# Kernel optimization log

Measured on AMD Instinct MI355X. Metric: run time of the kernel, lower is better.

## Reference

```python
import jax, jax.numpy as jnp
import numpy as np

DIM = 128
HEADS = 4
HD = DIM // HEADS  # 32
WS = 8             # search window (ws x ws candidates)
K = 16             # top-k neighbors kept
SCALE = HD ** -0.5


def _sepconv(x, w_dw, w_pw, b):
    # depthwise 3x3 ('SAME', reflect-free) + pointwise 1x1 with bias (SepConv2d)
    C = x.shape[1]
    y = jax.lax.conv_general_dilated(x, w_dw, (1, 1), 'SAME',
                                     feature_group_count=C,
                                     dimension_numbers=('NCHW', 'OIHW', 'NCHW'))
    return jnp.einsum('bchw,oc->bohw', y, w_pw) + b[None, :, None, None]


def _refl(i, n):
    # dnls reflect_bounds: mirror indices back into [0, n-1]
    i = jnp.where(i < 0, -i, i)
    return jnp.where(i >= n, 2 * (n - 1) - i, i)


def _neighbor_idx(T, H, W, ws):
    # flat pixel index of the ws*ws spatial candidates per query (wt=0: same frame)
    off = jnp.arange(ws) - ws // 2
    ni = _refl(jnp.arange(H)[:, None] + off[None, :], H)  # [H,ws]
    nj = _refl(jnp.arange(W)[:, None] + off[None, :], W)  # [W,ws]
    pix = ni[:, None, :, None] * W + nj[None, :, None, :]  # [H,W,ws,ws]
    idx = jnp.arange(T)[:, None, None, None, None] * (H * W) + pix[None]
    return idx.reshape(T * H * W, ws * ws).astype(jnp.int32)  # [Q,L]


def reference(vid, wq_dw, wq_pw, bq, wk_dw, wk_pw, bk, wv_dw, wv_pw, bv, proj_w, proj_b):
    B, T, C, H, W = vid.shape
    Q = T * H * W
    x = vid.reshape(B * T, C, H, W)
    # qkv conv projection; q pre-scaled as in get_qkv
    q = _sepconv(x, wq_dw, wq_pw, bq) * SCALE
    k = _sepconv(x, wk_dw, wk_pw, bk)
    v = _sepconv(x, wv_dw, wv_pw, bv)

    def heads(z):  # [B*T,C,H,W] -> [B,heads,Q,hd]
        return z.reshape(B, T, HEADS, HD, H, W).transpose(0, 2, 1, 4, 5, 3).reshape(B, HEADS, Q, HD)

    qh, kh, vh = heads(q), heads(k), heads(v)
    idx = _neighbor_idx(T, H, W, WS)            # [Q,L]
    kg = jnp.take(kh, idx, axis=2)              # [B,h,Q,L,hd] irregular gather
    dists = jnp.einsum('bhqd,bhqld->bhql', qh, kg)
    vals, args = jax.lax.top_k(dists, K)        # k-NN by prod distance
    attn = jax.nn.softmax(vals, axis=-1)        # run_softmax over k
    sel = jnp.take_along_axis(jnp.broadcast_to(idx[None, None], (B, HEADS) + idx.shape), args, axis=-1)
    vsel = jnp.take_along_axis(vh, sel.reshape(B, HEADS, Q * K)[..., None], axis=2).reshape(B, HEADS, Q, K, HD)
    out = jnp.einsum('bhqk,bhqkd->bhqd', attn, vsel)   # wpsum (ps=pt=1)
    out = out.transpose(0, 2, 1, 3).reshape(B, Q, C)   # merge heads: (h c)
    y = out @ proj_w.T + proj_b                        # nn.Linear proj
    # fold: ps=1, stride0=1 -> zvid==1, pure reshape back to video
    return y.reshape(B, T, H, W, C).transpose(0, 1, 4, 2, 3)


def setup_inputs() -> dict:
    key = jax.random.key(0)
    ks = jax.random.split(key, 12)
    s = 0.02
    return {
        'vid': jax.random.normal(ks[0], (1, 2, DIM, 96, 96), jnp.float32),
        'wq_dw': jax.random.normal(ks[1], (DIM, 1, 3, 3), jnp.float32) * s,
        'wq_pw': jax.random.normal(ks[2], (DIM, DIM), jnp.float32) * s,
        'bq': jax.random.normal(ks[3], (DIM,), jnp.float32) * s,
        'wk_dw': jax.random.normal(ks[4], (DIM, 1, 3, 3), jnp.float32) * s,
        'wk_pw': jax.random.normal(ks[5], (DIM, DIM), jnp.float32) * s,
        'bk': jax.random.normal(ks[6], (DIM,), jnp.float32) * s,
        'wv_dw': jax.random.normal(ks[7], (DIM, 1, 3, 3), jnp.float32) * s,
        'wv_pw': jax.random.normal(ks[8], (DIM, DIM), jnp.float32) * s,
        'bv': jax.random.normal(ks[9], (DIM,), jnp.float32) * s,
        'proj_w': jax.random.normal(ks[10], (DIM, DIM), jnp.float32) * s,
        'proj_b': jax.random.normal(ks[11], (DIM,), jnp.float32) * s,
    }
```

## Files before the change

kernel.cpp:

```cpp
#include <hip/hip_runtime.h>
#include <math.h>

#define TT 2
#define CH 128
#define HH 96
#define WW 96
#define HWS 9216
#define QTOT 18432
#define QC (QTOT*CH)
#define HD 32
#define KTOP 16
#define SCALE 0.17677669529663687f

#define SEG 16
#define PR 8
#define PC 23
#define PSTRIDE 36

typedef __attribute__((ext_vector_type(8))) short short8;
typedef __attribute__((ext_vector_type(4))) float floatx4;

__device__ __forceinline__ unsigned short f2bf(float f) {
    union { float f; unsigned u; } x; x.f = f;
    unsigned r = x.u + 0x7fffu + ((x.u >> 16) & 1u);
    return (unsigned short)(r >> 16);
}
__device__ __forceinline__ float bf2f(unsigned short h) {
    return __uint_as_float(((unsigned)h) << 16);
}

__device__ __forceinline__ int refl(int x, int n) {
    x = x < 0 ? -x : x;
    return x >= n ? 2 * (n - 1) - x : x;
}

__global__ __launch_bounds__(256) void dwcvt_kernel(
    const float* __restrict__ x,
    const float* __restrict__ wq, const float* __restrict__ wk, const float* __restrict__ wv,
    unsigned short* __restrict__ qk_hi,
    unsigned short* __restrict__ qk_lo,
    unsigned short* __restrict__ v_bf)
{
    int t = threadIdx.x;
    int pl = t & 63;
    int cg = __builtin_amdgcn_readfirstlane(t >> 6);
    int p  = blockIdx.x * 64 + pl;
    int c0 = blockIdx.y * 32 + cg * 8;
    int hw = p % HWS;
    int tt = p / HWS;
    int i = hw / WW, j = hw % WW;

    unsigned qh[4], ql[4], kh[4], kl[4], vh[4];
#pragma unroll
    for (int ic = 0; ic < 8; ic += 2) {
        float sv[3][2];
#pragma unroll
        for (int u = 0; u < 2; u++) {
            int c = c0 + ic + u;
            const float* xp = x + (size_t)(tt * CH + c) * HWS;
            float w0[9], w1[9], w2[9];
#pragma unroll
            for (int r = 0; r < 9; r++) {
                w0[r] = wq[c * 9 + r]; w1[r] = wk[c * 9 + r]; w2[r] = wv[c * 9 + r];
            }
            float s0 = 0.f, s1 = 0.f, s2 = 0.f;
#pragma unroll
            for (int r = 0; r < 3; r++) {
                int ii = i + r - 1;
                if (ii < 0 || ii >= HH) continue;
#pragma unroll
                for (int ss = 0; ss < 3; ss++) {
                    int jj = j + ss - 1;
                    if (jj < 0 || jj >= WW) continue;
                    float xv = xp[ii * WW + jj];
                    s0 += xv * w0[r * 3 + ss];
                    s1 += xv * w1[r * 3 + ss];
                    s2 += xv * w2[r * 3 + ss];
                }
            }
            sv[0][u] = s0; sv[1][u] = s1; sv[2][u] = s2;
        }
        int w = ic >> 1;
        unsigned short h0 = f2bf(sv[0][0]), h1 = f2bf(sv[0][1]);
        qh[w] = h0 | ((unsigned)h1 << 16);
        ql[w] = f2bf(sv[0][0] - bf2f(h0)) | ((unsigned)f2bf(sv[0][1] - bf2f(h1)) << 16);
        h0 = f2bf(sv[1][0]); h1 = f2bf(sv[1][1]);
        kh[w] = h0 | ((unsigned)h1 << 16);
        kl[w] = f2bf(sv[1][0] - bf2f(h0)) | ((unsigned)f2bf(sv[1][1] - bf2f(h1)) << 16);
        vh[w] = f2bf(sv[2][0]) | ((unsigned)f2bf(sv[2][1]) << 16);
    }
    size_t off = (size_t)p * CH + c0;
    uint4 pk;
    pk.x = qh[0]; pk.y = qh[1]; pk.z = qh[2]; pk.w = qh[3];
    *(uint4*)(qk_hi + off) = pk;
    pk.x = ql[0]; pk.y = ql[1]; pk.z = ql[2]; pk.w = ql[3];
    *(uint4*)(qk_lo + off) = pk;
    pk.x = kh[0]; pk.y = kh[1]; pk.z = kh[2]; pk.w = kh[3];
    *(uint4*)(qk_hi + (size_t)QC + off) = pk;
    pk.x = kl[0]; pk.y = kl[1]; pk.z = kl[2]; pk.w = kl[3];
    *(uint4*)(qk_lo + (size_t)QC + off) = pk;
    pk.x = vh[0]; pk.y = vh[1]; pk.z = vh[2]; pk.w = vh[3];
    *(uint4*)(v_bf + off) = pk;
}

__global__ __launch_bounds__(256) void qk_mfma(
    const unsigned short* __restrict__ Ahi,
    const unsigned short* __restrict__ Alo,
    const float* __restrict__ wq_pw, const float* __restrict__ wk_pw,
    const float* __restrict__ bq, const float* __restrict__ bk,
    float* __restrict__ qkf)
{
    int sel = blockIdx.y;
    const float* W = sel ? wk_pw : wq_pw;
    const float* bias = sel ? bk : bq;
    float scale = sel ? 1.f : SCALE;
    const unsigned short* ah = Ahi + (size_t)sel * QC;
    const unsigned short* al = Alo + (size_t)sel * QC;
    float* O = qkf + (size_t)sel * QC;

    __shared__ unsigned short Wh[128 * 136];
    __shared__ unsigned short Wl[128 * 136];
    int t = threadIdx.x;
#pragma unroll
    for (int r = 0; r < 16; r++) {
        int lin = r * 256 + t;
        int o = lin >> 5, cq = lin & 31;
        float4 w4 = *(const float4*)(W + o * CH + cq * 4);
        unsigned short hx = f2bf(w4.x), hy = f2bf(w4.y), hz = f2bf(w4.z), hw = f2bf(w4.w);
        unsigned short lx = f2bf(w4.x - bf2f(hx)), ly = f2bf(w4.y - bf2f(hy));
        unsigned short lz = f2bf(w4.z - bf2f(hz)), lw = f2bf(w4.w - bf2f(hw));
        uint2 pk;
        pk.x = hx | ((unsigned)hy << 16); pk.y = hz | ((unsigned)hw << 16);
        *(uint2*)(&Wh[o * 136 + cq * 4]) = pk;
        pk.x = lx | ((unsigned)ly << 16); pk.y = lz | ((unsigned)lw << 16);
        *(uint2*)(&Wl[o * 136 + cq * 4]) = pk;
    }
    __syncthreads();
    int wv = t >> 6, lane = t & 63;
    int m = lane & 15, quad = lane >> 4;
    int p0 = blockIdx.x * 64;
    int o0 = wv * 32;
    float bb[2];
#pragma unroll
    for (int ot = 0; ot < 2; ot++) bb[ot] = bias[o0 + ot * 16 + m];
    floatx4 acc[4][2];
#pragma unroll
    for (int i = 0; i < 4; i++)
#pragma unroll
        for (int j = 0; j < 2; j++) acc[i][j] = (floatx4){0.f, 0.f, 0.f, 0.f};
#pragma unroll
    for (int kc = 0; kc < 4; kc++) {
        short8 avh[4], avl[4], bh[2], bl[2];
#pragma unroll
        for (int pt = 0; pt < 4; pt++) {
            size_t base = (size_t)(p0 + pt * 16 + m) * CH + kc * 32 + quad * 8;
            avh[pt] = *(const short8*)(ah + base);
            avl[pt] = *(const short8*)(al + base);
        }
#pragma unroll
        for (int ot = 0; ot < 2; ot++) {
            int lidx = (o0 + ot * 16 + m) * 136 + kc * 32 + quad * 8;
            bh[ot] = *(const short8*)(&Wh[lidx]);
            bl[ot] = *(const short8*)(&Wl[lidx]);
        }
#pragma unroll
        for (int pt = 0; pt < 4; pt++)
#pragma unroll
            for (int ot = 0; ot < 2; ot++) {
                acc[pt][ot] = __builtin_amdgcn_mfma_f32_16x16x32_bf16(avh[pt], bh[ot], acc[pt][ot], 0, 0, 0);
                acc[pt][ot] = __builtin_amdgcn_mfma_f32_16x16x32_bf16(avh[pt], bl[ot], acc[pt][ot], 0, 0, 0);
                acc[pt][ot] = __builtin_amdgcn_mfma_f32_16x16x32_bf16(avl[pt], bh[ot], acc[pt][ot], 0, 0, 0);
            }
    }
#pragma unroll
    for (int pt = 0; pt < 4; pt++)
#pragma unroll
        for (int ot = 0; ot < 2; ot++)
#pragma unroll
            for (int reg = 0; reg < 4; reg++) {
                int p = p0 + pt * 16 + quad * 4 + reg;
                O[(size_t)p * CH + o0 + ot * 16 + m] = (acc[pt][ot][reg] + bb[ot]) * scale;
            }
}

__global__ __launch_bounds__(256) void vgemm_mfma(
    const unsigned short* __restrict__ A,
    const float* __restrict__ W,
    const float* __restrict__ bias,
    float* __restrict__ O)
{
    __shared__ unsigned short Ws[128 * 136];
    int t = threadIdx.x;
#pragma unroll
    for (int r = 0; r < 16; r++) {
        int lin = r * 256 + t;
        int o = lin >> 5, cq = lin & 31;
        float4 w4 = *(const float4*)(W + o * CH + cq * 4);
        uint2 pk;
        pk.x = f2bf(w4.x) | ((unsigned)f2bf(w4.y) << 16);
        pk.y = f2bf(w4.z) | ((unsigned)f2bf(w4.w) << 16);
        *(uint2*)(&Ws[o * 136 + cq * 4]) = pk;
    }
    __syncthreads();
    int wv = t >> 6, lane = t & 63;
    int m = lane & 15, quad = lane >> 4;
    int p0 = blockIdx.x * 64;
    int o0 = wv * 32;
    float bb[2];
#pragma unroll
    for (int ot = 0; ot < 2; ot++) bb[ot] = bias[o0 + ot * 16 + m];
    floatx4 acc[4][2];
#pragma unroll
    for (int i = 0; i < 4; i++)
#pragma unroll
        for (int j = 0; j < 2; j++) acc[i][j] = (floatx4){0.f, 0.f, 0.f, 0.f};
#pragma unroll
    for (int kc = 0; kc < 4; kc++) {
        short8 a[4], b[2];
#pragma unroll
        for (int pt = 0; pt < 4; pt++)
            a[pt] = *(const short8*)(A + (size_t)(p0 + pt * 16 + m) * CH + kc * 32 + quad * 8);
#pragma unroll
        for (int ot = 0; ot < 2; ot++)
            b[ot] = *(const short8*)(&Ws[(o0 + ot * 16 + m) * 136 + kc * 32 + quad * 8]);
#pragma unroll
        for (int pt = 0; pt < 4; pt++)
#pragma unroll
            for (int ot = 0; ot < 2; ot++)
                acc[pt][ot] = __builtin_amdgcn_mfma_f32_16x16x32_bf16(a[pt], b[ot], acc[pt][ot], 0, 0, 0);
    }
#pragma unroll
    for (int pt = 0; pt < 4; pt++)
#pragma unroll
        for (int ot = 0; ot < 2; ot++)
#pragma unroll
            for (int reg = 0; reg < 4; reg++) {
                int p = p0 + pt * 16 + quad * 4 + reg;
                O[(size_t)p * CH + o0 + ot * 16 + m] = acc[pt][ot][reg] + bb[ot];
            }
}

__global__ __launch_bounds__(256) void attn_kernel(
    const float* __restrict__ q,
    const float* __restrict__ k,
    const float* __restrict__ v,
    unsigned short* __restrict__ att)
{
    __shared__ float kp[PR * PC * PSTRIDE];
    int h = blockIdx.y;
    int seg = blockIdx.x;
    int qj0 = (seg % (WW / SEG)) * SEG;
    int qi = (seg / (WW / SEG)) % HH;
    int tt = seg / ((WW / SEG) * HH);
    int t = threadIdx.x;

#pragma unroll
    for (int r = 0; r < 6; r++) {
        int f = r * 256 + t;
        if (f < PR * PC * 8) {
            int pix = f >> 3, d4 = f & 7;
            int ci = pix / PC, cj = pix - ci * PC;
            int gi = refl(qi + ci - 4, HH);
            int gj = refl(qj0 + cj - 4, WW);
            int gp = tt * HWS + gi * WW + gj;
            *(float4*)(&kp[pix * PSTRIDE + d4 * 4]) =
                *(const float4*)(k + (size_t)gp * CH + h * HD + d4 * 4);
        }
    }
    __syncthreads();

    int wv = t >> 6, lane = t & 63;
    int ci = lane >> 3, cjo = lane & 7;
    int di = ci - 4, dj = cjo - 4;
    int rowoff = tt * HWS + refl(qi + di, HH) * WW;
    const int d = lane & (HD - 1);
    const unsigned long long below = (1ull << lane) - 1ull;

    for (int ql = wv * 4; ql < wv * 4 + 4; ql++) {
        int qj = qj0 + ql;
        int p = tt * HWS + qi * WW + qj;
        const float* qp = q + (size_t)p * CH + h * HD;
        const float* kr = &kp[(ci * PC + ql + cjo) * PSTRIDE];
        float dist = 0.f;
#pragma unroll
        for (int dd = 0; dd < 8; dd++) {
            float4 qv = *(const float4*)(qp + dd * 4);
            float4 kv = *(const float4*)(kr + dd * 4);
            dist += qv.x * kv.x + qv.y * kv.y + qv.z * kv.z + qv.w * kv.w;
        }
        int cpix = rowoff + refl(qj + dj, WW);

        unsigned u = __float_as_uint(dist);
        unsigned key = (u & 0x80000000u) ? ~u : (u | 0x80000000u);

        unsigned prefix = 0u;
        int need = KTOP;
#pragma unroll
        for (int bit = 31; bit >= 0; --bit) {
            unsigned hi = (prefix >> bit) | 1u;
            unsigned long long b = __ballot((key >> bit) == hi);
            int cnt = __popcll(b);
            bool take = cnt >= need;
            prefix = take ? (prefix | (1u << bit)) : prefix;
            need = take ? need : need - cnt;
        }
        bool isEq = (key == prefix);
        unsigned long long eqm = __ballot(isEq);
        int rk = __popcll(eqm & below);
        bool selb = (key > prefix) || (isEq && rk < need);
        unsigned long long selm = __ballot(selb);

        float e = selb ? __expf(dist) : 0.f;

        float acc = 0.f, denom = 0.f;
        unsigned long long m0 = selm;
#pragma unroll
        for (int r = 0; r < KTOP; r++) {
            int s0 = __builtin_ctzll(m0); m0 &= m0 - 1ull;
            float a0 = __uint_as_float((unsigned)__builtin_amdgcn_readlane((int)__float_as_uint(e), s0));
            int p0 = __builtin_amdgcn_readlane(cpix, s0);
            denom += a0;
            acc += a0 * v[(size_t)p0 * CH + h * HD + d];
        }
        if (lane < HD)
            att[(size_t)p * CH + h * HD + lane] = f2bf(acc / denom);
    }
}

__global__ __launch_bounds__(256) void proj_mfma(
    const unsigned short* __restrict__ A,
    const float* __restrict__ W,
    const float* __restrict__ bias,
    float* __restrict__ out)
{
    __shared__ unsigned short Ws[128 * 136];
    int t = threadIdx.x;
#pragma unroll
    for (int r = 0; r < 16; r++) {
        int lin = r * 256 + t;
        int o = lin >> 5, cq = lin & 31;
        float4 w4 = *(const float4*)(W + o * CH + cq * 4);
        uint2 pk;
        pk.x = f2bf(w4.x) | ((unsigned)f2bf(w4.y) << 16);
        pk.y = f2bf(w4.z) | ((unsigned)f2bf(w4.w) << 16);
        *(uint2*)(&Ws[o * 136 + cq * 4]) = pk;
    }
    __syncthreads();
    int wv = t >> 6, lane = t & 63;
    int m = lane & 15, quad = lane >> 4;
    int p0 = blockIdx.x * 64;
    int o0 = wv * 32;
    float bb[2][4];
#pragma unroll
    for (int ot = 0; ot < 2; ot++)
#pragma unroll
        for (int reg = 0; reg < 4; reg++) bb[ot][reg] = bias[o0 + ot * 16 + quad * 4 + reg];
    floatx4 acc[2][4];
#pragma unroll
    for (int i = 0; i < 2; i++)
#pragma unroll
        for (int j = 0; j < 4; j++) acc[i][j] = (floatx4){0.f, 0.f, 0.f, 0.f};
#pragma unroll
    for (int kc = 0; kc < 4; kc++) {
        short8 a[2], b[4];
#pragma unroll
        for (int ot = 0; ot < 2; ot++)
            a[ot] = *(const short8*)(&Ws[(o0 + ot * 16 + m) * 136 + kc * 32 + quad * 8]);
#pragma unroll
        for (int pt = 0; pt < 4; pt++)
            b[pt] = *(const short8*)(A + (size_t)(p0 + pt * 16 + m) * CH + kc * 32 + quad * 8);
#pragma unroll
        for (int ot = 0; ot < 2; ot++)
#pragma unroll
            for (int pt = 0; pt < 4; pt++)
                acc[ot][pt] = __builtin_amdgcn_mfma_f32_16x16x32_bf16(a[ot], b[pt], acc[ot][pt], 0, 0, 0);
    }
    int tt = p0 / HWS;
    int hwb = p0 - tt * HWS;
#pragma unroll
    for (int ot = 0; ot < 2; ot++)
#pragma unroll
        for (int pt = 0; pt < 4; pt++)
#pragma unroll
            for (int reg = 0; reg < 4; reg++) {
                int o = o0 + ot * 16 + quad * 4 + reg;
                int hw = hwb + pt * 16 + m;
                out[((size_t)(tt * CH + o)) * HWS + hw] = acc[ot][pt][reg] + bb[ot][reg];
            }
}

extern "C" void kernel_launch(void* const* d_in, const int* in_sizes, int n_in,
                              void* d_out, int out_size, void* d_ws, size_t ws_size,
                              hipStream_t stream) {
    const float* vid    = (const float*)d_in[0];
    const float* wq_dw  = (const float*)d_in[1];
    const float* wq_pw  = (const float*)d_in[2];
    const float* bq     = (const float*)d_in[3];
    const float* wk_dw  = (const float*)d_in[4];
    const float* wk_pw  = (const float*)d_in[5];
    const float* bk     = (const float*)d_in[6];
    const float* wv_dw  = (const float*)d_in[7];
    const float* wv_pw  = (const float*)d_in[8];
    const float* bv     = (const float*)d_in[9];
    const float* proj_w = (const float*)d_in[10];
    const float* proj_b = (const float*)d_in[11];
    float* out = (float*)d_out;

    float* qkf = (float*)d_ws;
    float* v_f32 = qkf + (size_t)2 * QC;
    unsigned short* qk_hi = (unsigned short*)(v_f32 + (size_t)QC);
    unsigned short* qk_lo = qk_hi + (size_t)2 * QC;
    unsigned short* v_bf = qk_lo + (size_t)2 * QC;
    unsigned short* att_bf = v_bf;

    dwcvt_kernel<<<dim3(QTOT / 64, 4), 256, 0, stream>>>(
        vid, wq_dw, wk_dw, wv_dw, qk_hi, qk_lo, v_bf);
    qk_mfma<<<dim3(QTOT / 64, 2), 256, 0, stream>>>(qk_hi, qk_lo, wq_pw, wk_pw, bq, bk, qkf);
    vgemm_mfma<<<QTOT / 64, 256, 0, stream>>>(v_bf, wv_pw, bv, v_f32);
    attn_kernel<<<dim3(TT * HH * (WW / SEG), 4), 256, 0, stream>>>(
        qkf, qkf + (size_t)QC, v_f32, att_bf);
    proj_mfma<<<QTOT / 64, 256, 0, stream>>>(att_bf, proj_w, proj_b, out);
}
```

Before: 206.0 us.

## Fuse V projection into QK GEMM and projection into attention kernel

Merges the V pointwise GEMM into the Q/K GEMM launch as a third grid slice, with a fourth slice pre-converting proj weights to bf16. V is now stored in bf16 in a per-head [h][Q][32] layout, which halves gather traffic and makes the 16 neighbor reads per query contiguous. The attention kernel loops over all four heads per block, keeps the attended row in LDS, and runs the output projection with MFMA directly, removing the att buffer round trip and a launch. In exchange each attention block does four times the serial work with fewer blocks, reloads K tiles per head with extra barriers, and reads proj weights from global memory instead of LDS.

```diff
diff --git a/kernel.cpp b/kernel.cpp
--- a/kernel.cpp
+++ b/kernel.cpp
@@ -50,7 +50,7 @@
     int tt = p / HWS;
     int i = hw / WW, j = hw % WW;
 
-    unsigned qh[4], ql[4], kh[4], kl[4], vh[4];
+    unsigned qh[4], ql[4], kh[4], kl[4], vh4[4];
 #pragma unroll
     for (int ic = 0; ic < 8; ic += 2) {
         float sv[3][2];
@@ -87,7 +87,7 @@
         h0 = f2bf(sv[1][0]); h1 = f2bf(sv[1][1]);
         kh[w] = h0 | ((unsigned)h1 << 16);
         kl[w] = f2bf(sv[1][0] - bf2f(h0)) | ((unsigned)f2bf(sv[1][1] - bf2f(h1)) << 16);
-        vh[w] = f2bf(sv[2][0]) | ((unsigned)f2bf(sv[2][1]) << 16);
+        vh4[w] = f2bf(sv[2][0]) | ((unsigned)f2bf(sv[2][1]) << 16);
     }
     size_t off = (size_t)p * CH + c0;
     uint4 pk;
@@ -99,18 +99,91 @@
     *(uint4*)(qk_hi + (size_t)QC + off) = pk;
     pk.x = kl[0]; pk.y = kl[1]; pk.z = kl[2]; pk.w = kl[3];
     *(uint4*)(qk_lo + (size_t)QC + off) = pk;
-    pk.x = vh[0]; pk.y = vh[1]; pk.z = vh[2]; pk.w = vh[3];
+    pk.x = vh4[0]; pk.y = vh4[1]; pk.z = vh4[2]; pk.w = vh4[3];
     *(uint4*)(v_bf + off) = pk;
 }
 
-__global__ __launch_bounds__(256) void qk_mfma(
+__global__ __launch_bounds__(256) void qkv_mfma(
     const unsigned short* __restrict__ Ahi,
     const unsigned short* __restrict__ Alo,
+    const unsigned short* __restrict__ Avb,
     const float* __restrict__ wq_pw, const float* __restrict__ wk_pw,
-    const float* __restrict__ bq, const float* __restrict__ bk,
-    float* __restrict__ qkf)
+    const float* __restrict__ wv_pw, const float* __restrict__ proj_w,
+    const float* __restrict__ bq, const float* __restrict__ bk, const float* __restrict__ bv,
+    float* __restrict__ qkf,
+    unsigned short* __restrict__ vh,
+    unsigned short* __restrict__ wp_bf)
 {
+    __shared__ unsigned short WhS[128 * 136];
+    __shared__ unsigned short WlS[128 * 136];
     int sel = blockIdx.y;
+    int t = threadIdx.x;
+
+    if (sel == 3) {
+        if (blockIdx.x < 16) {
+            int idx = blockIdx.x * 256 + t;
+            float4 w4 = *(const float4*)(proj_w + idx * 4);
+            uint2 pk;
+            pk.x = f2bf(w4.x) | ((unsigned)f2bf(w4.y) << 16);
+            pk.y = f2bf(w4.z) | ((unsigned)f2bf(w4.w) << 16);
+            *(uint2*)(wp_bf + idx * 4) = pk;
+        }
+        return;
+    }
+
+    int wv = t >> 6, lane = t & 63;
+    int m = lane & 15, quad = lane >> 4;
+    int p0 = blockIdx.x * 64;
+    int o0 = wv * 32;
+
+    if (sel == 2) {
+#pragma unroll
+        for (int r = 0; r < 16; r++) {
+            int lin = r * 256 + t;
+            int o = lin >> 5, cq = lin & 31;
+            float4 w4 = *(const float4*)(wv_pw + o * CH + cq * 4);
+            uint2 pk;
+            pk.x = f2bf(w4.x) | ((unsigned)f2bf(w4.y) << 16);
+            pk.y = f2bf(w4.z) | ((unsigned)f2bf(w4.w) << 16);
+            *(uint2*)(&WhS[o * 136 + cq * 4]) = pk;
+        }
+        __syncthreads();
+        float bb[2];
+#pragma unroll
+        for (int ot = 0; ot < 2; ot++) bb[ot] = bv[o0 + ot * 16 + m];
+        floatx4 acc[4][2];
+#pragma unroll
+        for (int i = 0; i < 4; i++)
+#pragma unroll
+            for (int j = 0; j < 2; j++) acc[i][j] = (floatx4){0.f, 0.f, 0.f, 0.f};
+#pragma unroll
+        for (int kc = 0; kc < 4; kc++) {
+            short8 a[4], b[2];
+#pragma unroll
+            for (int pt = 0; pt < 4; pt++)
+                a[pt] = *(const short8*)(Avb + (size_t)(p0 + pt * 16 + m) * CH + kc * 32 + quad * 8);
+#pragma unroll
+            for (int ot = 0; ot < 2; ot++)
+                b[ot] = *(const short8*)(&WhS[(o0 + ot * 16 + m) * 136 + kc * 32 + quad * 8]);
+#pragma unroll
+            for (int pt = 0; pt < 4; pt++)
+#pragma unroll
+                for (int ot = 0; ot < 2; ot++)
+                    acc[pt][ot] = __builtin_amdgcn_mfma_f32_16x16x32_bf16(a[pt], b[ot], acc[pt][ot], 0, 0, 0);
+        }
+        unsigned short* vhh = vh + (size_t)wv * QTOT * 32;
+#pragma unroll
+        for (int pt = 0; pt < 4; pt++)
+#pragma unroll
+            for (int ot = 0; ot < 2; ot++)
+#pragma unroll
+                for (int reg = 0; reg < 4; reg++) {
+                    int p = p0 + pt * 16 + quad * 4 + reg;
+                    vhh[(size_t)p * 32 + ot * 16 + m] = f2bf(acc[pt][ot][reg] + bb[ot]);
+                }
+        return;
+    }
+
     const float* W = sel ? wk_pw : wq_pw;
     const float* bias = sel ? bk : bq;
     float scale = sel ? 1.f : SCALE;
@@ -118,9 +191,6 @@
     const unsigned short* al = Alo + (size_t)sel * QC;
     float* O = qkf + (size_t)sel * QC;
 
-    __shared__ unsigned short Wh[128 * 136];
-    __shared__ unsigned short Wl[128 * 136];
-    int t = threadIdx.x;
 #pragma unroll
     for (int r = 0; r < 16; r++) {
         int lin = r * 256 + t;
@@ -131,15 +201,11 @@
         unsigned short lz = f2bf(w4.z - bf2f(hz)), lw = f2bf(w4.w - bf2f(hw));
         uint2 pk;
         pk.x = hx | ((unsigned)hy << 16); pk.y = hz | ((unsigned)hw << 16);
-        *(uint2*)(&Wh[o * 136 + cq * 4]) = pk;
+        *(uint2*)(&WhS[o * 136 + cq * 4]) = pk;
         pk.x = lx | ((unsigned)ly << 16); pk.y = lz | ((unsigned)lw << 16);
-        *(uint2*)(&Wl[o * 136 + cq * 4]) = pk;
+        *(uint2*)(&WlS[o * 136 + cq * 4]) = pk;
     }
     __syncthreads();
-    int wv = t >> 6, lane = t & 63;
-    int m = lane & 15, quad = lane >> 4;
-    int p0 = blockIdx.x * 64;
-    int o0 = wv * 32;
     float bb[2];
 #pragma unroll
     for (int ot = 0; ot < 2; ot++) bb[ot] = bias[o0 + ot * 16 + m];
@@ -160,8 +226,8 @@
 #pragma unroll
         for (int ot = 0; ot < 2; ot++) {
             int lidx = (o0 + ot * 16 + m) * 136 + kc * 32 + quad * 8;
-            bh[ot] = *(const short8*)(&Wh[lidx]);
-            bl[ot] = *(const short8*)(&Wl[lidx]);
+            bh[ot] = *(const short8*)(&WhS[lidx]);
+            bl[ot] = *(const short8*)(&WlS[lidx]);
         }
 #pragma unroll
         for (int pt = 0; pt < 4; pt++)
@@ -183,92 +249,22 @@
             }
 }
 
-__global__ __launch_bounds__(256) void vgemm_mfma(
-    const unsigned short* __restrict__ A,
-    const float* __restrict__ W,
-    const float* __restrict__ bias,
-    float* __restrict__ O)
-{
-    __shared__ unsigned short Ws[128 * 136];
-    int t = threadIdx.x;
-#pragma unroll
-    for (int r = 0; r < 16; r++) {
-        int lin = r * 256 + t;
-        int o = lin >> 5, cq = lin & 31;
-        float4 w4 = *(const float4*)(W + o * CH + cq * 4);
-        uint2 pk;
-        pk.x = f2bf(w4.x) | ((unsigned)f2bf(w4.y) << 16);
-        pk.y = f2bf(w4.z) | ((unsigned)f2bf(w4.w) << 16);
-        *(uint2*)(&Ws[o * 136 + cq * 4]) = pk;
-    }
-    __syncthreads();
-    int wv = t >> 6, lane = t & 63;
-    int m = lane & 15, quad = lane >> 4;
-    int p0 = blockIdx.x * 64;
-    int o0 = wv * 32;
-    float bb[2];
-#pragma unroll
-    for (int ot = 0; ot < 2; ot++) bb[ot] = bias[o0 + ot * 16 + m];
-    floatx4 acc[4][2];
-#pragma unroll
-    for (int i = 0; i < 4; i++)
-#pragma unroll
-        for (int j = 0; j < 2; j++) acc[i][j] = (floatx4){0.f, 0.f, 0.f, 0.f};
-#pragma unroll
-    for (int kc = 0; kc < 4; kc++) {
-        short8 a[4], b[2];
-#pragma unroll
-        for (int pt = 0; pt < 4; pt++)
-            a[pt] = *(const short8*)(A + (size_t)(p0 + pt * 16 + m) * CH + kc * 32 + quad * 8);
-#pragma unroll
-        for (int ot = 0; ot < 2; ot++)
-            b[ot] = *(const short8*)(&Ws[(o0 + ot * 16 + m) * 136 + kc * 32 + quad * 8]);
-#pragma unroll
-        for (int pt = 0; pt < 4; pt++)
-#pragma unroll
-            for (int ot = 0; ot < 2; ot++)
-                acc[pt][ot] = __builtin_amdgcn_mfma_f32_16x16x32_bf16(a[pt], b[ot], acc[pt][ot], 0, 0, 0);
-    }
-#pragma unroll
-    for (int pt = 0; pt < 4; pt++)
-#pragma unroll
-        for (int ot = 0; ot < 2; ot++)
-#pragma unroll
-            for (int reg = 0; reg < 4; reg++) {
-                int p = p0 + pt * 16 + quad * 4 + reg;
-                O[(size_t)p * CH + o0 + ot * 16 + m] = acc[pt][ot][reg] + bb[ot];
-            }
-}
-
-__global__ __launch_bounds__(256) void attn_kernel(
+__global__ __launch_bounds__(256) void attnproj_kernel(
     const float* __restrict__ q,
     const float* __restrict__ k,
-    const float* __restrict__ v,
-    unsigned short* __restrict__ att)
+    const unsigned short* __restrict__ vh,
+    const unsigned short* __restrict__ wp,
+    const float* __restrict__ pb,
+    float* __restrict__ out)
 {
     __shared__ float kp[PR * PC * PSTRIDE];
-    int h = blockIdx.y;
-    int seg = blockIdx.x;
+    __shared__ unsigned short att_s[16 * 136];
+    int n = blockIdx.x;
+    int seg = (n & 7) * 144 + (n >> 3);
     int qj0 = (seg % (WW / SEG)) * SEG;
     int qi = (seg / (WW / SEG)) % HH;
     int tt = seg / ((WW / SEG) * HH);
     int t = threadIdx.x;
-
-#pragma unroll
-    for (int r = 0; r < 6; r++) {
-        int f = r * 256 + t;
-        if (f < PR * PC * 8) {
-            int pix = f >> 3, d4 = f & 7;
-            int ci = pix / PC, cj = pix - ci * PC;
-            int gi = refl(qi + ci - 4, HH);
-            int gj = refl(qj0 + cj - 4, WW);
-            int gp = tt * HWS + gi * WW + gj;
-            *(float4*)(&kp[pix * PSTRIDE + d4 * 4]) =
-                *(const float4*)(k + (size_t)gp * CH + h * HD + d4 * 4);
-        }
-    }
-    __syncthreads();
-
     int wv = t >> 6, lane = t & 63;
     int ci = lane >> 3, cjo = lane & 7;
     int di = ci - 4, dj = cjo - 4;
@@ -276,117 +272,104 @@
     const int d = lane & (HD - 1);
     const unsigned long long below = (1ull << lane) - 1ull;
 
-    for (int ql = wv * 4; ql < wv * 4 + 4; ql++) {
-        int qj = qj0 + ql;
-        int p = tt * HWS + qi * WW + qj;
-        const float* qp = q + (size_t)p * CH + h * HD;
-        const float* kr = &kp[(ci * PC + ql + cjo) * PSTRIDE];
-        float dist = 0.f;
-#pragma unroll
-        for (int dd = 0; dd < 8; dd++) {
-            float4 qv = *(const float4*)(qp + dd * 4);
-            float4 kv = *(const float4*)(kr + dd * 4);
-            dist += qv.x * kv.x + qv.y * kv.y + qv.z * kv.z + qv.w * kv.w;
-        }
-        int cpix = rowoff + refl(qj + dj, WW);
-
-        unsigned u = __float_as_uint(dist);
-        unsigned key = (u & 0x80000000u) ? ~u : (u | 0x80000000u);
-
-        unsigned prefix = 0u;
-        int need = KTOP;
-#pragma unroll
-        for (int bit = 31; bit >= 0; --bit) {
-            unsigned hi = (prefix >> bit) | 1u;
-            unsigned long long b = __ballot((key >> bit) == hi);
-            int cnt = __popcll(b);
-            bool take = cnt >= need;
-            prefix = take ? (prefix | (1u << bit)) : prefix;
-            need = take ? need : need - cnt;
-        }
-        bool isEq = (key == prefix);
-        unsigned long long eqm = __ballot(isEq);
-        int rk = __popcll(eqm & below);
-        bool selb = (key > prefix) || (isEq && rk < need);
-        unsigned long long selm = __ballot(selb);
-
-        float e = selb ? __expf(dist) : 0.f;
-
-        float acc = 0.f, denom = 0.f;
-        unsigned long long m0 = selm;
-#pragma unroll
-        for (int r = 0; r < KTOP; r++) {
-            int s0 = __builtin_ctzll(m0); m0 &= m0 - 1ull;
-            float a0 = __uint_as_float((unsigned)__builtin_amdgcn_readlane((int)__float_as_uint(e), s0));
-            int p0 = __builtin_amdgcn_readlane(cpix, s0);
-            denom += a0;
-            acc += a0 * v[(size_t)p0 * CH + h * HD + d];
-        }
-        if (lane < HD)
-            att[(size_t)p * CH + h * HD + lane] = f2bf(acc / denom);
-    }
-}
-
-__global__ __launch_bounds__(256) void proj_mfma(
-    const unsigned short* __restrict__ A,
-    const float* __restrict__ W,
-    const float* __restrict__ bias,
-    float* __restrict__ out)
-{
-    __shared__ unsigned short Ws[128 * 136];
-    int t = threadIdx.x;
-#pragma unroll
-    for (int r = 0; r < 16; r++) {
-        int lin = r * 256 + t;
-        int o = lin >> 5, cq = lin & 31;
-        float4 w4 = *(const float4*)(W + o * CH + cq * 4);
-        uint2 pk;
-        pk.x = f2bf(w4.x) | ((unsigned)f2bf(w4.y) << 16);
-        pk.y = f2bf(w4.z) | ((unsigned)f2bf(w4.w) << 16);
-        *(uint2*)(&Ws[o * 136 + cq * 4]) = pk;
+    for (int h = 0; h < 4; h++) {
+        if (h) __syncthreads();
+#pragma unroll
+        for (int r = 0; r < 6; r++) {
+            int f = r * 256 + t;
+            if (f < PR * PC * 8) {
+                int pix = f >> 3, d4 = f & 7;
+                int pci = pix / PC, pcj = pix - pci * PC;
+                int gi = refl(qi + pci - 4, HH);
+                int gj = refl(qj0 + pcj - 4, WW);
+                int gp = tt * HWS + gi * WW + gj;
+                *(float4*)(&kp[pix * PSTRIDE + d4 * 4]) =
+                    *(const float4*)(k + (size_t)gp * CH + h * HD + d4 * 4);
+            }
+        }
+        __syncthreads();
+
+        const unsigned short* vhh = vh + (size_t)h * QTOT * 32;
+        for (int ql = wv * 4; ql < wv * 4 + 4; ql++) {
+            int qj = qj0 + ql;
+            int p = tt * HWS + qi * WW + qj;
+            const float* qp = q + (size_t)p * CH + h * HD;
+            const float* kr = &kp[(ci * PC + ql + cjo) * PSTRIDE];
+            float dist = 0.f;
+#pragma unroll
+            for (int dd = 0; dd < 8; dd++) {
+                float4 qv = *(const float4*)(qp + dd * 4);
+                float4 kv = *(const float4*)(kr + dd * 4);
+                dist += qv.x * kv.x + qv.y * kv.y + qv.z * kv.z + qv.w * kv.w;
+            }
+            int cpix = rowoff + refl(qj + dj, WW);
+
+            unsigned u = __float_as_uint(dist);
+            unsigned key = (u & 0x80000000u) ? ~u : (u | 0x80000000u);
+
+            unsigned prefix = 0u;
+            int need = KTOP;
+#pragma unroll
+            for (int bit = 31; bit >= 0; --bit) {
+                unsigned hi = (prefix >> bit) | 1u;
+                unsigned long long b = __ballot((key >> bit) == hi);
+                int cnt = __popcll(b);
+                bool take = cnt >= need;
+                prefix = take ? (prefix | (1u << bit)) : prefix;
+                need = take ? need : need - cnt;
+            }
+            bool isEq = (key == prefix);
+            unsigned long long eqm = __ballot(isEq);
+            int rk = __popcll(eqm & below);
+            bool selb = (key > prefix) || (isEq && rk < need);
+            unsigned long long selm = __ballot(selb);
+
+            float e = selb ? __expf(dist) : 0.f;
+
+            float acc = 0.f, denom = 0.f;
+            unsigned long long m0 = selm;
+#pragma unroll
+            for (int r = 0; r < KTOP; r++) {
+                int s0 = __builtin_ctzll(m0); m0 &= m0 - 1ull;
+                float a0 = __uint_as_float((unsigned)__builtin_amdgcn_readlane((int)__float_as_uint(e), s0));
+                int pr = __builtin_amdgcn_readlane(cpix, s0);
+                denom += a0;
+                acc += a0 * bf2f(vhh[(size_t)pr * 32 + d]);
+            }
+            if (lane < HD)
+                att_s[ql * 136 + h * HD + lane] = f2bf(acc / denom);
+        }
     }
     __syncthreads();
-    int wv = t >> 6, lane = t & 63;
+
     int m = lane & 15, quad = lane >> 4;
-    int p0 = blockIdx.x * 64;
     int o0 = wv * 32;
     float bb[2][4];
 #pragma unroll
     for (int ot = 0; ot < 2; ot++)
 #pragma unroll
-        for (int reg = 0; reg < 4; reg++) bb[ot][reg] = bias[o0 + ot * 16 + quad * 4 + reg];
-    floatx4 acc[2][4];
-#pragma unroll
-    for (int i = 0; i < 2; i++)
-#pragma unroll
-        for (int j = 0; j < 4; j++) acc[i][j] = (floatx4){0.f, 0.f, 0.f, 0.f};
+        for (int reg = 0; reg < 4; reg++) bb[ot][reg] = pb[o0 + ot * 16 + quad * 4 + reg];
+    floatx4 pacc[2];
+#pragma unroll
+    for (int i = 0; i < 2; i++) pacc[i] = (floatx4){0.f, 0.f, 0.f, 0.f};
 #pragma unroll
     for (int kc = 0; kc < 4; kc++) {
-        short8 a[2], b[4];
-#pragma unroll
-        for (int ot = 0; ot < 2; ot++)
-            a[ot] = *(const short8*)(&Ws[(o0 + ot * 16 + m) * 136 + kc * 32 + quad * 8]);
-#pragma unroll
-        for (int pt = 0; pt < 4; pt++)
-            b[pt] = *(const short8*)(A + (size_t)(p0 + pt * 16 + m) * CH + kc * 32 + quad * 8);
-#pragma unroll
-        for (int ot = 0; ot < 2; ot++)
-#pragma unroll
-            for (int pt = 0; pt < 4; pt++)
-                acc[ot][pt] = __builtin_amdgcn_mfma_f32_16x16x32_bf16(a[ot], b[pt], acc[ot][pt], 0, 0, 0);
-    }
-    int tt = p0 / HWS;
-    int hwb = p0 - tt * HWS;
+        short8 a[2], b;
+        b = *(const short8*)(&att_s[m * 136 + kc * 32 + quad * 8]);
+#pragma unroll
+        for (int ot = 0; ot < 2; ot++) {
+            a[ot] = *(const short8*)(wp + (o0 + ot * 16 + m) * CH + kc * 32 + quad * 8);
+            pacc[ot] = __builtin_amdgcn_mfma_f32_16x16x32_bf16(a[ot], b, pacc[ot], 0, 0, 0);
+        }
+    }
+    int hw0 = qi * WW + qj0;
 #pragma unroll
     for (int ot = 0; ot < 2; ot++)
 #pragma unroll
-        for (int pt = 0; pt < 4; pt++)
-#pragma unroll
-            for (int reg = 0; reg < 4; reg++) {
-                int o = o0 + ot * 16 + quad * 4 + reg;
-                int hw = hwb + pt * 16 + m;
-                out[((size_t)(tt * CH + o)) * HWS + hw] = acc[ot][pt][reg] + bb[ot][reg];
-            }
+        for (int reg = 0; reg < 4; reg++) {
+            int o = o0 + ot * 16 + quad * 4 + reg;
+            out[((size_t)(tt * CH + o)) * HWS + hw0 + m] = pacc[ot][reg] + bb[ot][reg];
+        }
 }
 
 extern "C" void kernel_launch(void* const* d_in, const int* in_sizes, int n_in,
@@ -407,17 +390,17 @@
     float* out = (float*)d_out;
 
     float* qkf = (float*)d_ws;
-    float* v_f32 = qkf + (size_t)2 * QC;
-    unsigned short* qk_hi = (unsigned short*)(v_f32 + (size_t)QC);
+    unsigned short* vh = (unsigned short*)(qkf + (size_t)2 * QC);
+    unsigned short* qk_hi = vh + (size_t)QC;
     unsigned short* qk_lo = qk_hi + (size_t)2 * QC;
     unsigned short* v_bf = qk_lo + (size_t)2 * QC;
-    unsigned short* att_bf = v_bf;
+    unsigned short* wp_bf = v_bf + (size_t)QC;
 
     dwcvt_kernel<<<dim3(QTOT / 64, 4), 256, 0, stream>>>(
         vid, wq_dw, wk_dw, wv_dw, qk_hi, qk_lo, v_bf);
-    qk_mfma<<<dim3(QTOT / 64, 2), 256, 0, stream>>>(qk_hi, qk_lo, wq_pw, wk_pw, bq, bk, qkf);
-    vgemm_mfma<<<QTOT / 64, 256, 0, stream>>>(v_bf, wv_pw, bv, v_f32);
-    attn_kernel<<<dim3(TT * HH * (WW / SEG), 4), 256, 0, stream>>>(
-        qkf, qkf + (size_t)QC, v_f32, att_bf);
-    proj_mfma<<<QTOT / 64, 256, 0, stream>>>(att_bf, proj_w, proj_b, out);
-}
+    qkv_mfma<<<dim3(QTOT / 64, 4), 256, 0, stream>>>(
+        qk_hi, qk_lo, v_bf, wq_pw, wk_pw, wv_pw, proj_w,
+        bq, bk, bv, qkf, vh, wp_bf);
+    attnproj_kernel<<<TT * HH * (WW / SEG), 256, 0, stream>>>(
+        qkf, qkf + (size_t)QC, vh, wp_bf, proj_b, out);
+}
```

After: 216.0 us. 1.05x slower.

## Fuse V GEMM into QK kernel, store V as per-head bf16, swizzle attn blocks

Applied to the files above, without the earlier changes.

Merges the separate V pointwise GEMM into the QK MFMA kernel as a third grid slice, removing one launch. V is now written as bf16 in a head-major layout ([head][pixel][32]), so the attention gather reads one contiguous 64-byte row per neighbour instead of strided fp32 values. The attention grid index is also remapped so consecutive blocks are spread across rows, which may change L2 locality. V precision drops from fp32 to bf16, so the attention output is slightly less accurate.

```diff
diff --git a/kernel.cpp b/kernel.cpp
--- a/kernel.cpp
+++ b/kernel.cpp
@@ -50,7 +50,7 @@
     int tt = p / HWS;
     int i = hw / WW, j = hw % WW;
 
-    unsigned qh[4], ql[4], kh[4], kl[4], vh[4];
+    unsigned qh[4], ql[4], kh[4], kl[4], vh4[4];
 #pragma unroll
     for (int ic = 0; ic < 8; ic += 2) {
         float sv[3][2];
@@ -87,7 +87,7 @@
         h0 = f2bf(sv[1][0]); h1 = f2bf(sv[1][1]);
         kh[w] = h0 | ((unsigned)h1 << 16);
         kl[w] = f2bf(sv[1][0] - bf2f(h0)) | ((unsigned)f2bf(sv[1][1] - bf2f(h1)) << 16);
-        vh[w] = f2bf(sv[2][0]) | ((unsigned)f2bf(sv[2][1]) << 16);
+        vh4[w] = f2bf(sv[2][0]) | ((unsigned)f2bf(sv[2][1]) << 16);
     }
     size_t off = (size_t)p * CH + c0;
     uint4 pk;
@@ -99,18 +99,77 @@
     *(uint4*)(qk_hi + (size_t)QC + off) = pk;
     pk.x = kl[0]; pk.y = kl[1]; pk.z = kl[2]; pk.w = kl[3];
     *(uint4*)(qk_lo + (size_t)QC + off) = pk;
-    pk.x = vh[0]; pk.y = vh[1]; pk.z = vh[2]; pk.w = vh[3];
+    pk.x = vh4[0]; pk.y = vh4[1]; pk.z = vh4[2]; pk.w = vh4[3];
     *(uint4*)(v_bf + off) = pk;
 }
 
-__global__ __launch_bounds__(256) void qk_mfma(
+__global__ __launch_bounds__(256) void qkv_mfma(
     const unsigned short* __restrict__ Ahi,
     const unsigned short* __restrict__ Alo,
+    const unsigned short* __restrict__ Avb,
     const float* __restrict__ wq_pw, const float* __restrict__ wk_pw,
-    const float* __restrict__ bq, const float* __restrict__ bk,
-    float* __restrict__ qkf)
+    const float* __restrict__ wv_pw,
+    const float* __restrict__ bq, const float* __restrict__ bk, const float* __restrict__ bv,
+    float* __restrict__ qkf,
+    unsigned short* __restrict__ vh)
 {
+    __shared__ unsigned short WhS[128 * 136];
+    __shared__ unsigned short WlS[128 * 136];
     int sel = blockIdx.y;
+    int t = threadIdx.x;
+    int wv = t >> 6, lane = t & 63;
+    int m = lane & 15, quad = lane >> 4;
+    int p0 = blockIdx.x * 64;
+    int o0 = wv * 32;
+
+    if (sel == 2) {
+#pragma unroll
+        for (int r = 0; r < 16; r++) {
+            int lin = r * 256 + t;
+            int o = lin >> 5, cq = lin & 31;
+            float4 w4 = *(const float4*)(wv_pw + o * CH + cq * 4);
+            uint2 pk;
+            pk.x = f2bf(w4.x) | ((unsigned)f2bf(w4.y) << 16);
+            pk.y = f2bf(w4.z) | ((unsigned)f2bf(w4.w) << 16);
+            *(uint2*)(&WhS[o * 136 + cq * 4]) = pk;
+        }
+        __syncthreads();
+        float bb[2];
+#pragma unroll
+        for (int ot = 0; ot < 2; ot++) bb[ot] = bv[o0 + ot * 16 + m];
+        floatx4 acc[4][2];
+#pragma unroll
+        for (int i = 0; i < 4; i++)
+#pragma unroll
+            for (int j = 0; j < 2; j++) acc[i][j] = (floatx4){0.f, 0.f, 0.f, 0.f};
+#pragma unroll
+        for (int kc = 0; kc < 4; kc++) {
+            short8 a[4], b[2];
+#pragma unroll
+            for (int pt = 0; pt < 4; pt++)
+                a[pt] = *(const short8*)(Avb + (size_t)(p0 + pt * 16 + m) * CH + kc * 32 + quad * 8);
+#pragma unroll
+            for (int ot = 0; ot < 2; ot++)
+                b[ot] = *(const short8*)(&WhS[(o0 + ot * 16 + m) * 136 + kc * 32 + quad * 8]);
+#pragma unroll
+            for (int pt = 0; pt < 4; pt++)
+#pragma unroll
+                for (int ot = 0; ot < 2; ot++)
+                    acc[pt][ot] = __builtin_amdgcn_mfma_f32_16x16x32_bf16(a[pt], b[ot], acc[pt][ot], 0, 0, 0);
+        }
+        unsigned short* vhh = vh + (size_t)wv * QTOT * 32;
+#pragma unroll
+        for (int pt = 0; pt < 4; pt++)
+#pragma unroll
+            for (int ot = 0; ot < 2; ot++)
+#pragma unroll
+                for (int reg = 0; reg < 4; reg++) {
+                    int p = p0 + pt * 16 + quad * 4 + reg;
+                    vhh[(size_t)p * 32 + ot * 16 + m] = f2bf(acc[pt][ot][reg] + bb[ot]);
+                }
+        return;
+    }
+
     const float* W = sel ? wk_pw : wq_pw;
     const float* bias = sel ? bk : bq;
     float scale = sel ? 1.f : SCALE;
@@ -118,9 +177,6 @@
     const unsigned short* al = Alo + (size_t)sel * QC;
     float* O = qkf + (size_t)sel * QC;
 
-    __shared__ unsigned short Wh[128 * 136];
-    __shared__ unsigned short Wl[128 * 136];
-    int t = threadIdx.x;
 #pragma unroll
     for (int r = 0; r < 16; r++) {
         int lin = r * 256 + t;
@@ -131,15 +187,11 @@
         unsigned short lz = f2bf(w4.z - bf2f(hz)), lw = f2bf(w4.w - bf2f(hw));
         uint2 pk;
         pk.x = hx | ((unsigned)hy << 16); pk.y = hz | ((unsigned)hw << 16);
-        *(uint2*)(&Wh[o * 136 + cq * 4]) = pk;
+        *(uint2*)(&WhS[o * 136 + cq * 4]) = pk;
         pk.x = lx | ((unsigned)ly << 16); pk.y = lz | ((unsigned)lw << 16);
-        *(uint2*)(&Wl[o * 136 + cq * 4]) = pk;
+        *(uint2*)(&WlS[o * 136 + cq * 4]) = pk;
     }
     __syncthreads();
-    int wv = t >> 6, lane = t & 63;
-    int m = lane & 15, quad = lane >> 4;
-    int p0 = blockIdx.x * 64;
-    int o0 = wv * 32;
     float bb[2];
 #pragma unroll
     for (int ot = 0; ot < 2; ot++) bb[ot] = bias[o0 + ot * 16 + m];
@@ -160,8 +212,8 @@
 #pragma unroll
         for (int ot = 0; ot < 2; ot++) {
             int lidx = (o0 + ot * 16 + m) * 136 + kc * 32 + quad * 8;
-            bh[ot] = *(const short8*)(&Wh[lidx]);
-            bl[ot] = *(const short8*)(&Wl[lidx]);
+            bh[ot] = *(const short8*)(&WhS[lidx]);
+            bl[ot] = *(const short8*)(&WlS[lidx]);
         }
 #pragma unroll
         for (int pt = 0; pt < 4; pt++)
@@ -183,72 +235,16 @@
             }
 }
 
-__global__ __launch_bounds__(256) void vgemm_mfma(
-    const unsigned short* __restrict__ A,
-    const float* __restrict__ W,
-    const float* __restrict__ bias,
-    float* __restrict__ O)
-{
-    __shared__ unsigned short Ws[128 * 136];
-    int t = threadIdx.x;
-#pragma unroll
-    for (int r = 0; r < 16; r++) {
-        int lin = r * 256 + t;
-        int o = lin >> 5, cq = lin & 31;
-        float4 w4 = *(const float4*)(W + o * CH + cq * 4);
-        uint2 pk;
-        pk.x = f2bf(w4.x) | ((unsigned)f2bf(w4.y) << 16);
-        pk.y = f2bf(w4.z) | ((unsigned)f2bf(w4.w) << 16);
-        *(uint2*)(&Ws[o * 136 + cq * 4]) = pk;
-    }
-    __syncthreads();
-    int wv = t >> 6, lane = t & 63;
-    int m = lane & 15, quad = lane >> 4;
-    int p0 = blockIdx.x * 64;
-    int o0 = wv * 32;
-    float bb[2];
-#pragma unroll
-    for (int ot = 0; ot < 2; ot++) bb[ot] = bias[o0 + ot * 16 + m];
-    floatx4 acc[4][2];
-#pragma unroll
-    for (int i = 0; i < 4; i++)
-#pragma unroll
-        for (int j = 0; j < 2; j++) acc[i][j] = (floatx4){0.f, 0.f, 0.f, 0.f};
-#pragma unroll
-    for (int kc = 0; kc < 4; kc++) {
-        short8 a[4], b[2];
-#pragma unroll
-        for (int pt = 0; pt < 4; pt++)
-            a[pt] = *(const short8*)(A + (size_t)(p0 + pt * 16 + m) * CH + kc * 32 + quad * 8);
-#pragma unroll
-        for (int ot = 0; ot < 2; ot++)
-            b[ot] = *(const short8*)(&Ws[(o0 + ot * 16 + m) * 136 + kc * 32 + quad * 8]);
-#pragma unroll
-        for (int pt = 0; pt < 4; pt++)
-#pragma unroll
-            for (int ot = 0; ot < 2; ot++)
-                acc[pt][ot] = __builtin_amdgcn_mfma_f32_16x16x32_bf16(a[pt], b[ot], acc[pt][ot], 0, 0, 0);
-    }
-#pragma unroll
-    for (int pt = 0; pt < 4; pt++)
-#pragma unroll
-        for (int ot = 0; ot < 2; ot++)
-#pragma unroll
-            for (int reg = 0; reg < 4; reg++) {
-                int p = p0 + pt * 16 + quad * 4 + reg;
-                O[(size_t)p * CH + o0 + ot * 16 + m] = acc[pt][ot][reg] + bb[ot];
-            }
-}
-
 __global__ __launch_bounds__(256) void attn_kernel(
     const float* __restrict__ q,
     const float* __restrict__ k,
-    const float* __restrict__ v,
+    const unsigned short* __restrict__ vh,
     unsigned short* __restrict__ att)
 {
     __shared__ float kp[PR * PC * PSTRIDE];
     int h = blockIdx.y;
-    int seg = blockIdx.x;
+    int n = blockIdx.x;
+    int seg = (n & 7) * 144 + (n >> 3);
     int qj0 = (seg % (WW / SEG)) * SEG;
     int qi = (seg / (WW / SEG)) % HH;
     int tt = seg / ((WW / SEG) * HH);
@@ -275,6 +271,7 @@
     int rowoff = tt * HWS + refl(qi + di, HH) * WW;
     const int d = lane & (HD - 1);
     const unsigned long long below = (1ull << lane) - 1ull;
+    const unsigned short* vhh = vh + (size_t)h * QTOT * 32;
 
     for (int ql = wv * 4; ql < wv * 4 + 4; ql++) {
         int qj = qj0 + ql;
@@ -318,9 +315,9 @@
         for (int r = 0; r < KTOP; r++) {
             int s0 = __builtin_ctzll(m0); m0 &= m0 - 1ull;
             float a0 = __uint_as_float((unsigned)__builtin_amdgcn_readlane((int)__float_as_uint(e), s0));
-            int p0 = __builtin_amdgcn_readlane(cpix, s0);
+            int pr = __builtin_amdgcn_readlane(cpix, s0);
             denom += a0;
-            acc += a0 * v[(size_t)p0 * CH + h * HD + d];
+            acc += a0 * bf2f(vhh[(size_t)pr * 32 + d]);
         }
         if (lane < HD)
             att[(size_t)p * CH + h * HD + lane] = f2bf(acc / denom);
@@ -407,17 +404,17 @@
     float* out = (float*)d_out;
 
     float* qkf = (float*)d_ws;
-    float* v_f32 = qkf + (size_t)2 * QC;
-    unsigned short* qk_hi = (unsigned short*)(v_f32 + (size_t)QC);
+    unsigned short* vh = (unsigned short*)(qkf + (size_t)2 * QC);
+    unsigned short* qk_hi = vh + (size_t)QC;
     unsigned short* qk_lo = qk_hi + (size_t)2 * QC;
     unsigned short* v_bf = qk_lo + (size_t)2 * QC;
     unsigned short* att_bf = v_bf;
 
     dwcvt_kernel<<<dim3(QTOT / 64, 4), 256, 0, stream>>>(
         vid, wq_dw, wk_dw, wv_dw, qk_hi, qk_lo, v_bf);
-    qk_mfma<<<dim3(QTOT / 64, 2), 256, 0, stream>>>(qk_hi, qk_lo, wq_pw, wk_pw, bq, bk, qkf);
-    vgemm_mfma<<<QTOT / 64, 256, 0, stream>>>(v_bf, wv_pw, bv, v_f32);
+    qkv_mfma<<<dim3(QTOT / 64, 3), 256, 0, stream>>>(
+        qk_hi, qk_lo, v_bf, wq_pw, wk_pw, wv_pw, bq, bk, bv, qkf, vh);
     attn_kernel<<<dim3(TT * HH * (WW / SEG), 4), 256, 0, stream>>>(
-        qkf, qkf + (size_t)QC, v_f32, att_bf);
+        qkf, qkf + (size_t)QC, vh, att_bf);
     proj_mfma<<<QTOT / 64, 256, 0, stream>>>(att_bf, proj_w, proj_b, out);
 }
```

Measured after the change: 203.6 us. No clear change (-1.2%).
